# Optimization experiments

Measured on AMD Instinct MI355X. Metric: run time of the kernel, lower is better.

The kernel has to match this reference:

```python
import jax, jax.numpy as jnp
import numpy as np
from jax import lax

DN = ('NCHW', 'OIHW', 'NCHW')

def _pconv(x, mask, w, b):
    # Partial conv: conv(masked x) rescaled by K/valid_count; mask_next = valid>0.
    C = x.shape[1]
    k = w.shape[2]
    p = k // 2
    K = C * k * k
    xm = x * mask  # mask broadcasts over channels (== repeat in torch code)
    xp = jnp.pad(xm, ((0, 0), (0, 0), (p, p), (p, p)))  # zeros, as in F.pad value=0
    y = lax.conv_general_dilated(xp, w, (1, 1), 'VALID', dimension_numbers=DN)
    # mask padded with 1.0 (as in the torch module), summed over kxk window
    mp = jnp.pad(mask, ((0, 0), (0, 0), (p, p), (p, p)), constant_values=1.0)
    ones_k = jnp.ones((1, 1, k, k), x.dtype)
    msum = lax.conv_general_dilated(mp, ones_k, (1, 1), 'VALID', dimension_numbers=DN)
    valid = C * msum  # [N,1,H,W] = sum over all K unfold rows
    scale = K / jnp.maximum(valid, 1.0)
    y = y * scale + b[None, :, None, None]
    no_valid = valid <= 0.0
    y = jnp.where(no_valid, 0.0, y)
    mask_next = (~no_valid).astype(x.dtype)
    return y, mask_next

def _bn_relu(x, gamma, beta, eps=1e-5):
    # training-mode BatchNorm2d: per-batch biased stats over (N,H,W)
    mu = jnp.mean(x, axis=(0, 2, 3), keepdims=True)
    var = jnp.var(x, axis=(0, 2, 3), keepdims=True)
    xn = (x - mu) * lax.rsqrt(var + eps)
    return jax.nn.relu(xn * gamma[None, :, None, None] + beta[None, :, None, None])

def _pool21(x):
    # MaxPool2d(kernel=(2,1), stride=(2,1))
    N, C, H, W = x.shape
    return x.reshape(N, C, H // 2, 2, W).max(axis=3)

def setup_inputs() -> dict:
    key = jax.random.key(0)
    ks = iter(jax.random.split(key, 32))
    base = 80
    def kaiming(k, shape):
        fan_in = shape[1] * shape[2] * shape[3]
        return jax.random.normal(k, shape, jnp.float32) * np.sqrt(2.0 / fan_in)
    def lin(k, out, inp):
        bound = 1.0 / np.sqrt(inp)
        kw, kb = jax.random.split(k)
        W = jax.random.uniform(kw, (out, inp), jnp.float32, -bound, bound)
        b = jax.random.uniform(kb, (out,), jnp.float32, -bound, bound)
        return W, b
    x = jax.random.normal(next(ks), (16, 2, 256, 128), jnp.float32)
    d = {'x': x}
    chans = [(1, base), (base, 2 * base), (2 * base, 4 * base), (4 * base, 8 * base)]
    for i, (ci, co) in enumerate(chans, 1):
        d[f'w{i}'] = kaiming(next(ks), (co, ci, 3, 3))
        d[f'b{i}'] = jnp.zeros((co,), jnp.float32)
        d[f'g{i}'] = jnp.ones((co,), jnp.float32)
        d[f'be{i}'] = jnp.zeros((co,), jnp.float32)
    d['fw1'], d['fb1'] = lin(next(ks), 256, 8 * base)
    d['fw2'], d['fb2'] = lin(next(ks), 128, 256)
    d['hw'], d['hb'] = lin(next(ks), 1, 128)
    return d

def reference(x, w1, b1, g1, be1, w2, b2, g2, be2, w3, b3, g3, be3,
              w4, b4, g4, be4, fw1, fb1, fw2, fb2, hw, hb):
    data = x[:, 0:1, :, :]
    mask = jnp.clip(x[:, 1:2, :, :], 0.0, 1.0)
    h, m = data, mask
    for w, b, g, be in ((w1, b1, g1, be1), (w2, b2, g2, be2),
                        (w3, b3, g3, be3), (w4, b4, g4, be4)):
        h, m = _pconv(h, m, w, b)
        h = _bn_relu(h, g, be)
        h = _pool21(h)
        m = _pool21(m)
    feat = jnp.mean(h, axis=(2, 3))  # GAP -> [N, 8*base]
    z = jax.nn.relu(feat @ fw1.T + fb1)
    z = jax.nn.relu(z @ fw2.T + fb2)  # dropout = identity (eval)
    return jax.nn.sigmoid(z @ hw.T + hb)[:, 0]
```

## Files before the change

kernel.cpp:

```cpp
#include <hip/hip_runtime.h>
#include <math.h>

#define NB 16
#define WD 128

typedef __bf16 bf16_t;
typedef __bf16 bf16x8 __attribute__((ext_vector_type(8)));
typedef __bf16 bf16x4 __attribute__((ext_vector_type(4)));
typedef float f32x4 __attribute__((ext_vector_type(4)));

__device__ inline float rowsum16(float v) {
  int t;
  t = __builtin_amdgcn_update_dpp(0, __float_as_int(v), 0x111, 0xf, 0xf, true);
  v += __int_as_float(t);
  t = __builtin_amdgcn_update_dpp(0, __float_as_int(v), 0x112, 0xf, 0xf, true);
  v += __int_as_float(t);
  t = __builtin_amdgcn_update_dpp(0, __float_as_int(v), 0x114, 0xf, 0xf, true);
  v += __int_as_float(t);
  t = __builtin_amdgcn_update_dpp(0, __float_as_int(v), 0x118, 0xf, 0xf, true);
  v += __int_as_float(t);
  return v;
}

__device__ inline float sum64(float v) {
  v = rowsum16(v);
  int t = __builtin_amdgcn_update_dpp(0, __float_as_int(v), 0x142, 0xf, 0xf, true);
  v += __int_as_float(t);
  t = __builtin_amdgcn_update_dpp(0, __float_as_int(v), 0x143, 0xf, 0xf, true);
  v += __int_as_float(t);
  return v;
}

__global__ void zero_k(float* __restrict__ p, int n) {
  int i = blockIdx.x * 256 + threadIdx.x;
  if (i < n) p[i] = 0.f;
}

__global__ void zb_k(bf16_t* __restrict__ out, int Hp, int NCB) {
  int trow = NB * 2 * NCB * 576;
  int tcol = NB * Hp * NCB * 8;
  int i = blockIdx.x * 256 + threadIdx.x;
  bf16x8 z = (bf16x8)(bf16_t)0.f;
  if (i < trow) {
    int e = i % 576;
    int t = i / 576;
    int cb = t % NCB;
    t /= NCB;
    int rsel = t & 1;
    int n = t >> 1;
    int row = rsel ? (Hp + 1) : 0;
    *(bf16x8*)&out[(((size_t)n * (Hp + 2) + row) * NCB + cb) * 4608 + e * 8] = z;
  } else if (i < trow + tcol) {
    int k = i - trow;
    int j = k & 7;
    int t = k >> 3;
    int cb = t % NCB;
    t /= NCB;
    int row = (t % Hp) + 1;
    int n = t / Hp;
    size_t base = (((size_t)n * (Hp + 2) + row) * NCB + cb) * 4608;
    size_t off = (j < 4) ? (size_t)(j * 128) : (size_t)(4096 + (j - 4) * 128 + 8);
    *(bf16x8*)&out[base + off] = z;
  }
}

__global__ void split_k(const float* __restrict__ x, float* __restrict__ data,
                        float* __restrict__ mask) {
  const int HW = 256 * 128;
  int i = blockIdx.x * 256 + threadIdx.x;
  if (i >= NB * HW) return;
  int n = i / HW, rem = i % HW;
  data[i] = x[(size_t)(n * 2) * HW + rem];
  float mv = x[(size_t)(n * 2 + 1) * HW + rem];
  mask[i] = fminf(fmaxf(mv, 0.f), 1.f);
}

__global__ void maskscale2_k(const float* __restrict__ m, float* __restrict__ scale,
                             float* __restrict__ mnext, float* __restrict__ mpool,
                             int H, float Ci) {
  int Hp = H / 2;
  int i = blockIdx.x * 256 + threadIdx.x;
  int tot = NB * Hp * WD;
  if (i >= tot) return;
  int x = i % WD;
  int t = i / WD;
  int yo = t % Hp;
  int n = t / Hp;
  const float* mn_ = m + (size_t)n * H * WD;
  float mx[2];
#pragma unroll
  for (int r = 0; r < 2; ++r) {
    int y = 2 * yo + r;
    float s = 0.f;
#pragma unroll
    for (int dy = -1; dy <= 1; dy++) {
      int yy = y + dy;
#pragma unroll
      for (int dx = -1; dx <= 1; dx++) {
        int xx = x + dx;
        float v = 1.0f;
        if (yy >= 0 && yy < H && xx >= 0 && xx < WD) v = mn_[yy * WD + xx];
        s += v;
      }
    }
    float valid = Ci * s;
    int p = (n * H + y) * WD + x;
    scale[p] = (9.0f * Ci) / fmaxf(valid, 1.0f);
    float mnx = (valid <= 0.0f) ? 0.f : 1.f;
    mnext[p] = mnx;
    mx[r] = mnx;
  }
  mpool[((size_t)n * Hp + yo) * WD + x] = fmaxf(mx[0], mx[1]);
}

#define PROWS 2048
#define P1STR 4096
#define PCO 640

__global__ void pconv1p_k(const float* __restrict__ data,
                          const float* __restrict__ mask,
                          const float* __restrict__ w, const float* __restrict__ b,
                          const float* __restrict__ scale,
                          const float* __restrict__ mnext,
                          bf16_t* __restrict__ yp, float* __restrict__ part) {
  __shared__ float ws[720];
  __shared__ float bs[80];
  for (int i = threadIdx.x; i < 720; i += 256) ws[i] = w[i];
  if (threadIdx.x < 80) bs[threadIdx.x] = b[threadIdx.x];
  __syncthreads();
  const int H = 256, Hp = 128;
  int p2 = blockIdx.x * 256 + threadIdx.x;
  int x = p2 % WD;
  int t = p2 / WD;
  int yo = t % Hp;
  int n = t / Hp;
  const float* dn = data + (size_t)n * H * WD;
  const float* mn = mask + (size_t)n * H * WD;
  float vin[4][3];
#pragma unroll
  for (int r4 = 0; r4 < 4; ++r4) {
    int yv = 2 * yo - 1 + r4;
#pragma unroll
    for (int dx = 0; dx < 3; ++dx) {
      int xv = x - 1 + dx;
      float u = 0.f;
      if (yv >= 0 && yv < H && xv >= 0 && xv < WD)
        u = dn[yv * WD + xv] * mn[yv * WD + xv];
      vin[r4][dx] = u;
    }
  }
  int p0 = (n * H + 2 * yo) * WD + x;
  float sc0 = scale[p0], mx0 = mnext[p0];
  float sc1 = scale[p0 + WD], mx1 = mnext[p0 + WD];
  bf16_t* outp = yp + ((size_t)(n * Hp + yo) * WD + x) * 80;
  const int wave = threadIdx.x >> 6;
  const int lane = threadIdx.x & 63;
  const int row = blockIdx.x * 4 + wave;
#pragma unroll
  for (int c8 = 0; c8 < 10; ++c8) {
    bf16x8 o;
    float sA[8], qA[8];
#pragma unroll
    for (int j = 0; j < 8; ++j) {
      int co = c8 * 8 + j;
      float s0 = 0.f, s1 = 0.f;
#pragma unroll
      for (int dy = 0; dy < 3; ++dy)
#pragma unroll
        for (int dx = 0; dx < 3; ++dx) {
          float wv = ws[co * 9 + dy * 3 + dx];
          s0 += wv * vin[dy][dx];
          s1 += wv * vin[dy + 1][dx];
        }
      bf16_t o0 = (bf16_t)((s0 * sc0 + bs[co]) * mx0);
      bf16_t o1 = (bf16_t)((s1 * sc1 + bs[co]) * mx1);
      float f0 = (float)o0, f1 = (float)o1;
      sA[j] = f0 + f1;
      qA[j] = f0 * f0 + f1 * f1;
      o[j] = (bf16_t)fmaxf(f0, f1);
    }
    *(bf16x8*)(outp + c8 * 8) = o;
#pragma unroll
    for (int j = 0; j < 8; ++j) {
      sA[j] = sum64(sA[j]);
      qA[j] = sum64(qA[j]);
    }
    if (lane == 63) {
#pragma unroll
      for (int j = 0; j < 8; ++j) {
        int co = c8 * 8 + j;
        part[(size_t)co * P1STR + row] = sA[j];
        part[(size_t)PCO * PROWS + (size_t)co * P1STR + row] = qA[j];
      }
    }
  }
}

__global__ void wtrans_k(const float* __restrict__ w, bf16_t* __restrict__ wt2,
                         int Ci, int Co, int NCB, int Co_pad) {
  int idx = blockIdx.x * 256 + threadIdx.x;
  int total = 9 * NCB * Co_pad * 32;
  if (idx >= total) return;
  int j = idx & 7;
  int rest = idx >> 3;
  int co = rest % Co_pad;
  int rest2 = rest / Co_pad;
  int g = rest2 & 3;
  int rest3 = rest2 >> 2;
  int cb = rest3 % NCB;
  int tap = rest3 / NCB;
  int ci = cb * 32 + g * 8 + j;
  float v = 0.f;
  if (co < Co && ci < Ci) v = w[((size_t)co * Ci + ci) * 9 + tap];
  wt2[idx] = (bf16_t)v;
}

template <int MF>
__global__ __launch_bounds__(256, 2) void convmfma_t(
    const bf16_t* __restrict__ xmT, const bf16_t* __restrict__ wt2,
    const float* __restrict__ bias, const float* __restrict__ scale,
    const float* __restrict__ mnext, bf16_t* __restrict__ y,
    float* __restrict__ part, int H, int NCB, int Co, int Cop, int coOff) {
  __shared__ bf16_t Bb[2][4][4608];
  const int tid = threadIdx.x;
  const int lane = tid & 63;
  const int wave = tid >> 6;
  const int wm = wave >> 1;
  const int wn = wave & 1;
  const int g = lane >> 4;
  const int ln = lane & 15;
  constexpr int TILE = MF * 32;
  constexpr int EPS = TILE + 8;
  constexpr int NCO8 = TILE / 8;

  const int gx = gridDim.x;
  const int nwg = gx * (int)gridDim.y;
  const int orig = (int)blockIdx.y * gx + (int)blockIdx.x;
  const int wg = (orig & 7) * (nwg >> 3) + (orig >> 3);
  const int coTile = coOff + (wg % gx) * TILE;
  const int bx = wg / gx;
  const int Hh = H >> 1;
  const int n = bx / Hh, yp_ = bx % Hh;
  const int y0 = yp_ * 2;

  f32x4 acc[MF][8];
#pragma unroll
  for (int mf = 0; mf < MF; mf++)
#pragma unroll
    for (int nf = 0; nf < 8; nf++) acc[mf][nf] = (f32x4)(0.f);

  const size_t cbStride = 4608;
  const size_t rowStrideG = (size_t)NCB * cbStride;
  const size_t gRow0 = ((size_t)n * (H + 2) + y0) * rowStrideG;
  const size_t laneOff = (size_t)lane * 8;

  const size_t tapStrideA = (size_t)NCB * 4 * Cop * 8;
  const size_t cbStrideA = (size_t)4 * Cop * 8;
  const bf16_t* aLane = wt2 + ((size_t)g * Cop + coTile + wm * (MF * 16) + ln) * 8;

  int offdx[3];
#pragma unroll
  for (int dx = 0; dx < 3; ++dx) {
    int cx = ln + dx;
    offdx[dx] = ((cx & 15) * 8) + ((cx >> 4) * 512) + g * 128;
  }

  {
    const bf16_t* bsrc = xmT + gRow0;
    for (int c = wave; c < 36; c += 4) {
      int row = c / 9, chk = c - row * 9;
      __builtin_amdgcn_global_load_lds(
          (const __attribute__((address_space(1))) void*)(
              bsrc + (size_t)row * rowStrideG + chk * 512 + laneOff),
          (__attribute__((address_space(3))) void*)(&Bb[0][row][chk * 512]), 16, 0, 0);
    }
  }
  __syncthreads();

  int cur = 0;
  for (int cb = 0; cb < NCB; ++cb) {
    if (cb + 1 < NCB) {
      const bf16_t* bsrc = xmT + gRow0 + (size_t)(cb + 1) * cbStride;
      for (int c = wave; c < 36; c += 4) {
        int row = c / 9, chk = c - row * 9;
        __builtin_amdgcn_global_load_lds(
            (const __attribute__((address_space(1))) void*)(
                bsrc + (size_t)row * rowStrideG + chk * 512 + laneOff),
            (__attribute__((address_space(3))) void*)(&Bb[cur ^ 1][row][chk * 512]), 16,
            0, 0);
      }
    }
    const bf16_t* aCb = aLane + (size_t)cb * cbStrideA;
#pragma unroll
    for (int dy = 0; dy < 3; ++dy) {
      const bf16_t* brow = &Bb[cur][wn + dy][0];
#pragma unroll
      for (int dx = 0; dx < 3; ++dx) {
        const bf16_t* aTap = aCb + (size_t)(dy * 3 + dx) * tapStrideA;
        bf16x8 a[MF];
#pragma unroll
        for (int mf = 0; mf < MF; ++mf) a[mf] = *(const bf16x8*)(aTap + mf * 128);
        const bf16_t* bb = brow + offdx[dx];
#pragma unroll
        for (int nf = 0; nf < 8; ++nf) {
          bf16x8 b = *(const bf16x8*)(bb + nf * 512);
#pragma unroll
          for (int mf = 0; mf < MF; ++mf)
            acc[mf][nf] =
                __builtin_amdgcn_mfma_f32_16x16x32_bf16(a[mf], b, acc[mf][nf], 0, 0, 0);
        }
      }
    }
    __syncthreads();
    cur ^= 1;
  }

  const int yrowW = y0 + wn;
  const int pixBaseW = (n * H + yrowW) * WD;
  float scl[8], msk[8];
#pragma unroll
  for (int nf = 0; nf < 8; ++nf) {
    int x = nf * 16 + ln;
    scl[nf] = scale[pixBaseW + x];
    msk[nf] = mnext[pixBaseW + x];
  }
  float sA[4 * MF], qA[4 * MF];
#pragma unroll
  for (int i = 0; i < 4 * MF; ++i) { sA[i] = 0.f; qA[i] = 0.f; }
  bf16_t* ep = &Bb[0][0][0];
#pragma unroll
  for (int rp = 0; rp < 2; ++rp) {
    __syncthreads();
    if (wn == rp) {
#pragma unroll
      for (int mf = 0; mf < MF; ++mf) {
        int cbase = wm * (MF * 16) + mf * 16;
        f32x4 bias4 = *(const f32x4*)&bias[coTile + cbase + g * 4];
#pragma unroll
        for (int nf = 0; nf < 8; ++nf) {
          bf16x4 o;
#pragma unroll
          for (int r = 0; r < 4; ++r) {
            o[r] = (bf16_t)((acc[mf][nf][r] * scl[nf] + bias4[r]) * msk[nf]);
            float f = (float)o[r];
            sA[mf * 4 + r] += f;
            qA[mf * 4 + r] += f * f;
          }
          bf16_t* slot = &ep[(nf * 16 + ln) * EPS + cbase + g * 4];
          if (rp == 0) {
            *(bf16x4*)slot = o;
          } else {
            bf16x4 c0 = *(const bf16x4*)slot;
#pragma unroll
            for (int r = 0; r < 4; ++r)
              o[r] = (bf16_t)fmaxf((float)c0[r], (float)o[r]);
            *(bf16x4*)slot = o;
          }
        }
      }
    }
  }
  __syncthreads();
  {
    const size_t prow = ((size_t)n * Hh + yp_) * WD;
    for (int idx = tid; idx < 128 * NCO8; idx += 256) {
      int cgrp = idx % NCO8;
      int p = idx / NCO8;
      bf16x8 v = *(const bf16x8*)&ep[p * EPS + cgrp * 8];
      *(bf16x8*)&y[(prow + p) * Co + coTile + cgrp * 8] = v;
    }
  }

#pragma unroll
  for (int i = 0; i < 4 * MF; ++i) {
    sA[i] = rowsum16(sA[i]);
    qA[i] = rowsum16(qA[i]);
  }
  if (ln == 15) {
    const int row = bx * 2 + wn;
#pragma unroll
    for (int i = 0; i < 4 * MF; ++i) {
      int co = coTile + wm * (MF * 16) + (i >> 2) * 16 + g * 4 + (i & 3);
      part[(size_t)co * PROWS + row] = sA[i];
      part[(size_t)PCO * PROWS + (size_t)co * PROWS + row] = qA[i];
    }
  }
}

__global__ __launch_bounds__(256) void bnfin_r(const float* __restrict__ part,
                                               const float* __restrict__ g,
                                               const float* __restrict__ be,
                                               float* __restrict__ ab, int Co,
                                               int rows, int stride,
                                               float invCount) {
  int c = blockIdx.x;
  int tid = threadIdx.x;
  float s = 0.f, q = 0.f;
  for (int r = tid; r < rows; r += 256) {
    s += part[(size_t)c * stride + r];
    q += part[(size_t)PCO * PROWS + (size_t)c * stride + r];
  }
  __shared__ float rs[256], rq[256];
  rs[tid] = s;
  rq[tid] = q;
  __syncthreads();
  for (int off = 128; off > 0; off >>= 1) {
    if (tid < off) {
      rs[tid] += rs[tid + off];
      rq[tid] += rq[tid + off];
    }
    __syncthreads();
  }
  if (tid == 0) {
    float mean = rs[0] * invCount;
    float var = rq[0] * invCount - mean * mean;
    float rsq = rsqrtf(var + 1e-5f);
    float a = g[c] * rsq;
    ab[c] = a;
    ab[Co + c] = be[c] - mean * a;
  }
}

__global__ void bnpoolp_k(const bf16_t* __restrict__ yp, const float* __restrict__ ab,
                          const float* __restrict__ mp, bf16_t* __restrict__ out, int C,
                          int NCBn, int Hp) {
  int Cq = C / 8;
  int tid = blockIdx.x * 256 + threadIdx.x;
  int total = NB * Hp * WD * Cq;
  if (tid >= total) return;
  int c8 = tid % Cq;
  int t = tid / Cq;
  int x = t % WD;
  t /= WD;
  int yo = t % Hp;
  int n = t / Hp;
  int c = c8 * 8;
  const bf16_t* p0 = yp + ((size_t)((n * Hp + yo) * WD + x)) * C + c;
  float mpv = mp[(n * Hp + yo) * WD + x];
  bf16x8 v0 = *(const bf16x8*)p0;
  bf16x8 o;
#pragma unroll
  for (int j = 0; j < 8; ++j) {
    float a = ab[c + j], sh = ab[C + c + j];
    float f0 = (float)v0[j] * a + sh;
    o[j] = (bf16_t)(fmaxf(f0, 0.f) * mpv);
  }
  int cb = c >> 5;
  int gg = (c & 31) >> 3;
  int col = x + 1;
  int chk = col >> 4, lcol = col & 15;
  *(bf16x8*)&out[((((size_t)n * (Hp + 2) + yo + 1) * NCBn + cb) * 9 + chk) * 512 +
                 gg * 128 + lcol * 8] = o;
}

__global__ void bnfeatp_k(const bf16_t* __restrict__ yp, const float* __restrict__ ab,
                          float* __restrict__ feat) {
  int n = blockIdx.x, cc = blockIdx.y, yo = blockIdx.z;
  int c = cc * 128 + threadIdx.x;
  float a = ab[c], sh = ab[640 + c];
  float s = 0.f;
  for (int x = 0; x < WD; ++x) {
    size_t p0 = ((size_t)(n * 16 + yo) * WD + x) * 640 + c;
    float v = (float)yp[p0] * a + sh;
    s += fmaxf(v, 0.f);
  }
  atomicAdd(&feat[n * 640 + c], s * (1.f / 2048.f));
}

__global__ void fc1_k(const float* __restrict__ feat, const float* __restrict__ fw,
                      const float* __restrict__ fb, float* __restrict__ z1) {
  int n = blockIdx.x;
  int o = threadIdx.x;
  const float* f = feat + n * 640;
  const float* wr = fw + o * 640;
  float s = fb[o];
  for (int k = 0; k < 640; k++) s += f[k] * wr[k];
  z1[n * 256 + o] = fmaxf(s, 0.f);
}

__global__ void fc2h_k(const float* __restrict__ z1, const float* __restrict__ fw2,
                       const float* __restrict__ fb2, const float* __restrict__ hw,
                       const float* __restrict__ hb, float* __restrict__ out) {
  int n = blockIdx.x;
  int o = threadIdx.x;
  const float* zr = z1 + n * 256;
  const float* wr = fw2 + o * 256;
  float s = fb2[o];
  for (int k = 0; k < 256; k++) s += zr[k] * wr[k];
  s = fmaxf(s, 0.f) * hw[o];
#pragma unroll
  for (int off = 32; off >= 1; off >>= 1) s += __shfl_down(s, off, 64);
  __shared__ float red[2];
  if ((threadIdx.x & 63) == 0) red[threadIdx.x >> 6] = s;
  __syncthreads();
  if (threadIdx.x == 0) {
    float t = red[0] + red[1] + hb[0];
    out[n] = 1.f / (1.f + expf(-t));
  }
}

extern "C" void kernel_launch(void* const* d_in, const int* in_sizes, int n_in,
                              void* d_out, int out_size, void* d_ws, size_t ws_size,
                              hipStream_t stream) {
  const float* x = (const float*)d_in[0];
  const float* wgt[4] = {(const float*)d_in[1], (const float*)d_in[5],
                         (const float*)d_in[9], (const float*)d_in[13]};
  const float* bias[4] = {(const float*)d_in[2], (const float*)d_in[6],
                          (const float*)d_in[10], (const float*)d_in[14]};
  const float* gam[4] = {(const float*)d_in[3], (const float*)d_in[7],
                         (const float*)d_in[11], (const float*)d_in[15]};
  const float* bet[4] = {(const float*)d_in[4], (const float*)d_in[8],
                         (const float*)d_in[12], (const float*)d_in[16]};
  const float* fw1 = (const float*)d_in[17];
  const float* fb1 = (const float*)d_in[18];
  const float* fw2 = (const float*)d_in[19];
  const float* fb2 = (const float*)d_in[20];
  const float* hw = (const float*)d_in[21];
  const float* hb = (const float*)d_in[22];

  char* base = (char*)d_ws;
  size_t off = 0;
  auto alloc = [&](size_t bytes) {
    char* p = base + off;
    off += (bytes + 255) & ~(size_t)255;
    return p;
  };
  bf16_t* bufY = (bf16_t*)alloc(83886080);
  const size_t xmtElems = 28786688;
  bf16_t* xmT0 = (bf16_t*)alloc(xmtElems * 2);
  bf16_t* xmT1 = (bf16_t*)alloc(xmtElems * 2);
  bf16_t* wt2 = (bf16_t*)alloc(3686400);
  float* data = (float*)alloc(2097152);
  float* mask0 = (float*)alloc(2097152);
  float* mask1 = (float*)alloc(2097152);
  float* scaleB = (float*)alloc(2097152);
  float* mnextB = (float*)alloc(2097152);
  float* part = (float*)alloc((size_t)2 * 640 * 2048 * 4);
  float* bnab = (float*)alloc(5120);
  float* feat = (float*)alloc(40960);
  float* z1 = (float*)alloc(16384);

  zero_k<<<40, 256, 0, stream>>>(feat, 10240);

  split_k<<<(NB * 256 * 128 + 255) / 256, 256, 0, stream>>>(x, data, mask0);

  {
    int H = 256;
    int tot = NB * H * WD;
    maskscale2_k<<<(tot / 2 + 255) / 256, 256, 0, stream>>>(mask0, scaleB, mnextB,
                                                            mask1, H, 1.0f);
    pconv1p_k<<<tot / 2 / 256, 256, 0, stream>>>(data, mask0, wgt[0], bias[0], scaleB,
                                                 mnextB, bufY, part);
    bnfin_r<<<80, 256, 0, stream>>>(part, gam[0], bet[0], bnab, 80, P1STR, P1STR,
                                    1.0f / (NB * (float)H * WD));
    {
      int tz = NB * 2 * 3 * 576 + NB * 128 * 3 * 8;
      zb_k<<<(tz + 255) / 256, 256, 0, stream>>>(xmT0, 128, 3);
    }
    int totp = NB * 128 * WD * (80 / 8);
    bnpoolp_k<<<(totp + 255) / 256, 256, 0, stream>>>(bufY, bnab, mask1, xmT0, 80, 3,
                                                      128);
  }

  const int CiS[3] = {80, 160, 320};
  const int NCBS[3] = {3, 5, 10};
  const int CoS[3] = {160, 320, 640};
  const int HS[3] = {128, 64, 32};
  bf16_t* xin[3] = {xmT0, xmT1, xmT0};
  bf16_t* xout[3] = {xmT1, xmT0, nullptr};
  float* mIn[3] = {mask1, mask0, mask1};
  float* mOut[3] = {mask0, mask1, mask0 };

  for (int s = 0; s < 3; ++s) {
    int H = HS[s], Ci = CiS[s], NCB = NCBS[s], Co = CoS[s];
    int wtot = 9 * NCB * Co * 32;
    wtrans_k<<<(wtot + 255) / 256, 256, 0, stream>>>(wgt[s + 1], wt2, Ci, Co, NCB, Co);
    int tot = NB * H * WD;
    maskscale2_k<<<(tot / 2 + 255) / 256, 256, 0, stream>>>(mIn[s], scaleB, mnextB,
                                                            mOut[s], H, (float)Ci);
    int Hh2 = NB * (H / 2);
    int tiles = Co / 160;
    convmfma_t<5><<<dim3(tiles, Hh2), 256, 0, stream>>>(
        xin[s], wt2, bias[s + 1], scaleB, mnextB, bufY, part, H, NCB, Co, Co, 0);
    bnfin_r<<<Co, 256, 0, stream>>>(part, gam[s + 1], bet[s + 1], bnab, Co, NB * H,
                                    PROWS, 1.0f / (NB * (float)H * WD));
    if (s < 2) {
      int Hpn = H / 2, NCBn = NCBS[s + 1];
      int tz = NB * 2 * NCBn * 576 + NB * Hpn * NCBn * 8;
      zb_k<<<(tz + 255) / 256, 256, 0, stream>>>(xout[s], Hpn, NCBn);
      int totp = NB * Hpn * WD * (Co / 8);
      bnpoolp_k<<<(totp + 255) / 256, 256, 0, stream>>>(bufY, bnab, mOut[s], xout[s],
                                                        Co, NCBn, Hpn);
    } else {
      bnfeatp_k<<<dim3(16, 5, 16), 128, 0, stream>>>(bufY, bnab, feat);
    }
  }

  fc1_k<<<16, 256, 0, stream>>>(feat, fw1, fb1, z1);
  fc2h_k<<<16, 128, 0, stream>>>(z1, fw2, fb2, hw, hb, (float*)d_out);
}
```

Measured before the change: 654.7 us.

## Split waves by pixel columns and reuse weight fragments across both output rows

Each wave now computes both output rows for half the pixel columns instead of one row for all columns. Weight fragments for taps dy are loaded once and reused for both output rows, so A-operand loads drop and each LDS B row serves two accumulators. The 2x1 max-pool then happens in registers, removing the two-pass LDS epilogue and its barriers. The partial BN-stat rows are now indexed by column half rather than image row, which changes the row's meaning but keeps the sums correct.

Result: faster. 607.2 us (-7.3%).

```diff
diff --git a/kernel.cpp b/kernel.cpp
--- a/kernel.cpp
+++ b/kernel.cpp
@@ -226,7 +226,7 @@
   const int lane = tid & 63;
   const int wave = tid >> 6;
   const int wm = wave >> 1;
-  const int wn = wave & 1;
+  const int wp = wave & 1;
   const int g = lane >> 4;
   const int ln = lane & 15;
   constexpr int TILE = MF * 32;
@@ -243,11 +243,14 @@
   const int n = bx / Hh, yp_ = bx % Hh;
   const int y0 = yp_ * 2;
 
-  f32x4 acc[MF][8];
+  f32x4 acc0[MF][4], acc1[MF][4];
 #pragma unroll
   for (int mf = 0; mf < MF; mf++)
 #pragma unroll
-    for (int nf = 0; nf < 8; nf++) acc[mf][nf] = (f32x4)(0.f);
+    for (int nf = 0; nf < 4; nf++) {
+      acc0[mf][nf] = (f32x4)(0.f);
+      acc1[mf][nf] = (f32x4)(0.f);
+    }
 
   const size_t cbStride = 4608;
   const size_t rowStrideG = (size_t)NCB * cbStride;
@@ -262,7 +265,7 @@
 #pragma unroll
   for (int dx = 0; dx < 3; ++dx) {
     int cx = ln + dx;
-    offdx[dx] = ((cx & 15) * 8) + ((cx >> 4) * 512) + g * 128;
+    offdx[dx] = wp * 2048 + ((cx & 15) * 8) + ((cx >> 4) * 512) + g * 128;
   }
 
   {
@@ -292,72 +295,110 @@
     }
     const bf16_t* aCb = aLane + (size_t)cb * cbStrideA;
 #pragma unroll
-    for (int dy = 0; dy < 3; ++dy) {
-      const bf16_t* brow = &Bb[cur][wn + dy][0];
-#pragma unroll
-      for (int dx = 0; dx < 3; ++dx) {
-        const bf16_t* aTap = aCb + (size_t)(dy * 3 + dx) * tapStrideA;
-        bf16x8 a[MF];
-#pragma unroll
-        for (int mf = 0; mf < MF; ++mf) a[mf] = *(const bf16x8*)(aTap + mf * 128);
-        const bf16_t* bb = brow + offdx[dx];
-#pragma unroll
-        for (int nf = 0; nf < 8; ++nf) {
-          bf16x8 b = *(const bf16x8*)(bb + nf * 512);
+    for (int dx = 0; dx < 3; ++dx) {
+      bf16x8 a0[MF], a1[MF], a2[MF];
+      bf16x8 b[4];
+      {
+        const bf16_t* aT = aCb + (size_t)dx * tapStrideA;
+#pragma unroll
+        for (int mf = 0; mf < MF; ++mf) a0[mf] = *(const bf16x8*)(aT + mf * 128);
+        const bf16_t* bb = &Bb[cur][0][0] + offdx[dx];
+#pragma unroll
+        for (int nf = 0; nf < 4; ++nf) b[nf] = *(const bf16x8*)(bb + nf * 512);
+#pragma unroll
+        for (int nf = 0; nf < 4; ++nf)
 #pragma unroll
           for (int mf = 0; mf < MF; ++mf)
-            acc[mf][nf] =
-                __builtin_amdgcn_mfma_f32_16x16x32_bf16(a[mf], b, acc[mf][nf], 0, 0, 0);
-        }
+            acc0[mf][nf] =
+                __builtin_amdgcn_mfma_f32_16x16x32_bf16(a0[mf], b[nf], acc0[mf][nf], 0, 0, 0);
+      }
+      {
+        const bf16_t* aT = aCb + (size_t)(3 + dx) * tapStrideA;
+#pragma unroll
+        for (int mf = 0; mf < MF; ++mf) a1[mf] = *(const bf16x8*)(aT + mf * 128);
+        const bf16_t* bb = &Bb[cur][1][0] + offdx[dx];
+#pragma unroll
+        for (int nf = 0; nf < 4; ++nf) b[nf] = *(const bf16x8*)(bb + nf * 512);
+#pragma unroll
+        for (int nf = 0; nf < 4; ++nf)
+#pragma unroll
+          for (int mf = 0; mf < MF; ++mf)
+            acc0[mf][nf] =
+                __builtin_amdgcn_mfma_f32_16x16x32_bf16(a1[mf], b[nf], acc0[mf][nf], 0, 0, 0);
+#pragma unroll
+        for (int nf = 0; nf < 4; ++nf)
+#pragma unroll
+          for (int mf = 0; mf < MF; ++mf)
+            acc1[mf][nf] =
+                __builtin_amdgcn_mfma_f32_16x16x32_bf16(a0[mf], b[nf], acc1[mf][nf], 0, 0, 0);
+      }
+      {
+        const bf16_t* aT = aCb + (size_t)(6 + dx) * tapStrideA;
+#pragma unroll
+        for (int mf = 0; mf < MF; ++mf) a2[mf] = *(const bf16x8*)(aT + mf * 128);
+        const bf16_t* bb = &Bb[cur][2][0] + offdx[dx];
+#pragma unroll
+        for (int nf = 0; nf < 4; ++nf) b[nf] = *(const bf16x8*)(bb + nf * 512);
+#pragma unroll
+        for (int nf = 0; nf < 4; ++nf)
+#pragma unroll
+          for (int mf = 0; mf < MF; ++mf)
+            acc0[mf][nf] =
+                __builtin_amdgcn_mfma_f32_16x16x32_bf16(a2[mf], b[nf], acc0[mf][nf], 0, 0, 0);
+#pragma unroll
+        for (int nf = 0; nf < 4; ++nf)
+#pragma unroll
+          for (int mf = 0; mf < MF; ++mf)
+            acc1[mf][nf] =
+                __builtin_amdgcn_mfma_f32_16x16x32_bf16(a1[mf], b[nf], acc1[mf][nf], 0, 0, 0);
+      }
+      {
+        const bf16_t* bb = &Bb[cur][3][0] + offdx[dx];
+#pragma unroll
+        for (int nf = 0; nf < 4; ++nf) b[nf] = *(const bf16x8*)(bb + nf * 512);
+#pragma unroll
+        for (int nf = 0; nf < 4; ++nf)
+#pragma unroll
+          for (int mf = 0; mf < MF; ++mf)
+            acc1[mf][nf] =
+                __builtin_amdgcn_mfma_f32_16x16x32_bf16(a2[mf], b[nf], acc1[mf][nf], 0, 0, 0);
       }
     }
     __syncthreads();
     cur ^= 1;
   }
 
-  const int yrowW = y0 + wn;
-  const int pixBaseW = (n * H + yrowW) * WD;
-  float scl[8], msk[8];
-#pragma unroll
-  for (int nf = 0; nf < 8; ++nf) {
-    int x = nf * 16 + ln;
-    scl[nf] = scale[pixBaseW + x];
-    msk[nf] = mnext[pixBaseW + x];
+  const int pixBase0 = (n * H + y0) * WD;
+  float scl0[4], msk0[4], scl1[4], msk1[4];
+#pragma unroll
+  for (int nf = 0; nf < 4; ++nf) {
+    int x = wp * 64 + nf * 16 + ln;
+    scl0[nf] = scale[pixBase0 + x];
+    msk0[nf] = mnext[pixBase0 + x];
+    scl1[nf] = scale[pixBase0 + WD + x];
+    msk1[nf] = mnext[pixBase0 + WD + x];
   }
   float sA[4 * MF], qA[4 * MF];
 #pragma unroll
   for (int i = 0; i < 4 * MF; ++i) { sA[i] = 0.f; qA[i] = 0.f; }
   bf16_t* ep = &Bb[0][0][0];
 #pragma unroll
-  for (int rp = 0; rp < 2; ++rp) {
-    __syncthreads();
-    if (wn == rp) {
-#pragma unroll
-      for (int mf = 0; mf < MF; ++mf) {
-        int cbase = wm * (MF * 16) + mf * 16;
-        f32x4 bias4 = *(const f32x4*)&bias[coTile + cbase + g * 4];
-#pragma unroll
-        for (int nf = 0; nf < 8; ++nf) {
-          bf16x4 o;
-#pragma unroll
-          for (int r = 0; r < 4; ++r) {
-            o[r] = (bf16_t)((acc[mf][nf][r] * scl[nf] + bias4[r]) * msk[nf]);
-            float f = (float)o[r];
-            sA[mf * 4 + r] += f;
-            qA[mf * 4 + r] += f * f;
-          }
-          bf16_t* slot = &ep[(nf * 16 + ln) * EPS + cbase + g * 4];
-          if (rp == 0) {
-            *(bf16x4*)slot = o;
-          } else {
-            bf16x4 c0 = *(const bf16x4*)slot;
-#pragma unroll
-            for (int r = 0; r < 4; ++r)
-              o[r] = (bf16_t)fmaxf((float)c0[r], (float)o[r]);
-            *(bf16x4*)slot = o;
-          }
-        }
-      }
+  for (int mf = 0; mf < MF; ++mf) {
+    int cbase = wm * (MF * 16) + mf * 16;
+    f32x4 bias4 = *(const f32x4*)&bias[coTile + cbase + g * 4];
+#pragma unroll
+    for (int nf = 0; nf < 4; ++nf) {
+      bf16x4 o;
+#pragma unroll
+      for (int r = 0; r < 4; ++r) {
+        bf16_t v0 = (bf16_t)((acc0[mf][nf][r] * scl0[nf] + bias4[r]) * msk0[nf]);
+        bf16_t v1 = (bf16_t)((acc1[mf][nf][r] * scl1[nf] + bias4[r]) * msk1[nf]);
+        float f0 = (float)v0, f1 = (float)v1;
+        sA[mf * 4 + r] += f0 + f1;
+        qA[mf * 4 + r] += f0 * f0 + f1 * f1;
+        o[r] = (bf16_t)fmaxf(f0, f1);
+      }
+      *(bf16x4*)&ep[(wp * 64 + nf * 16 + ln) * EPS + cbase + g * 4] = o;
     }
   }
   __syncthreads();
@@ -377,7 +418,7 @@
     qA[i] = rowsum16(qA[i]);
   }
   if (ln == 15) {
-    const int row = bx * 2 + wn;
+    const int row = bx * 2 + wp;
 #pragma unroll
     for (int i = 0; i < 4 * MF; ++i) {
       int co = coTile + wm * (MF * 16) + (i >> 2) * 16 + g * 4 + (i & 3);
```
